# Optimization experiments

Hardware: AMD Instinct MI355X
Metric: run time of the kernel (lower is better)

The kernel has to match this reference:

```python
import jax, jax.numpy as jnp
import numpy as np

NUM_SAMPLES = 2048
MAX_AGENTS = 64
D_MODEL = 128
NUM_HEADS = 8


def setup_inputs() -> dict:
    key = jax.random.key(0)
    # deterministic ragged sizes: 1..64 repeating -> total = 32 * (64*65/2) = 66560
    agents = ((np.arange(NUM_SAMPLES) % MAX_AGENTS) + 1).astype(np.int32)
    total = int(agents.sum())
    k1, k2, k3 = jax.random.split(key, 3)
    s = 1.0 / np.sqrt(D_MODEL)
    return {
        "att_in": jax.random.normal(k1, (total, D_MODEL), jnp.float32),
        "in_proj_w": jax.random.uniform(k2, (3 * D_MODEL, D_MODEL), jnp.float32, -s, s),
        "in_proj_b": jnp.zeros((3 * D_MODEL,), jnp.float32),
        "out_proj_w": jax.random.uniform(k3, (D_MODEL, D_MODEL), jnp.float32, -s, s),
        "out_proj_b": jnp.zeros((D_MODEL,), jnp.float32),
        "agents_per_sample": jnp.asarray(agents),
    }


def reference(att_in, in_proj_w, in_proj_b, out_proj_w, out_proj_b, agents_per_sample):
    # agents_per_sample is static ragged metadata (host ints)
    agents = np.asarray(agents_per_sample)
    B = len(agents)
    A = int(agents.max())
    D = att_in.shape[-1]
    hd = D // NUM_HEADS

    # scatter ragged tokens into zero-padded [B, A, D]
    sample_ids = np.repeat(np.arange(B), agents)
    pos = np.concatenate([np.arange(n) for n in agents])
    padded = jnp.zeros((B, A, D), att_in.dtype).at[sample_ids, pos].set(att_in)
    key_valid = jnp.asarray(np.arange(A)[None, :] < agents[:, None])  # [B, A]

    # torch nn.MultiheadAttention math (eval mode, dropout=0)
    qkv = padded @ in_proj_w.T + in_proj_b  # [B, A, 3D]
    q, k, v = jnp.split(qkv, 3, axis=-1)
    q = q.reshape(B, A, NUM_HEADS, hd)
    k = k.reshape(B, A, NUM_HEADS, hd)
    v = v.reshape(B, A, NUM_HEADS, hd)

    scores = jnp.einsum("bqhd,bkhd->bhqk", q, k) / jnp.sqrt(jnp.asarray(hd, q.dtype))
    scores = jnp.where(key_valid[:, None, None, :], scores, jnp.asarray(-1e30, scores.dtype))
    attn = jax.nn.softmax(scores, axis=-1)

    out = jnp.einsum("bhqk,bkhd->bqhd", attn, v).reshape(B, A, D)
    out = out @ out_proj_w.T + out_proj_b

    # unpad: concatenation of the per-sample ragged outputs
    return out[sample_ids, pos]
```

## Files before the change

kernel.cpp:

```cpp
#include <hip/hip_runtime.h>

#define DM 128

typedef __attribute__((ext_vector_type(8))) __bf16 bf16x8;
typedef __attribute__((ext_vector_type(4))) float f32x4;

__device__ inline unsigned short f2bf(float f) {
    unsigned u = __float_as_uint(f);
    u += 0x7FFFu + ((u >> 16) & 1u);
    return (unsigned short)(u >> 16);
}

__global__ void prep(const int* __restrict__ agents, int B, int M,
                     const float* __restrict__ wqkv, const float* __restrict__ wout,
                     const float* __restrict__ x,
                     int* __restrict__ offs,
                     unsigned short* __restrict__ wqkv_bf,
                     unsigned short* __restrict__ wout_bf,
                     unsigned short* __restrict__ xbf) {
    if (blockIdx.x < 64) {
        int idx = (blockIdx.x * 256 + threadIdx.x) * 4;
        if (idx < 49152) {
            float4 v = *(const float4*)(wqkv + idx);
            ushort4 o;
            o.x = f2bf(v.x); o.y = f2bf(v.y); o.z = f2bf(v.z); o.w = f2bf(v.w);
            *(ushort4*)(wqkv_bf + idx) = o;
        } else {
            int j = idx - 49152;
            float4 v = *(const float4*)(wout + j);
            ushort4 o;
            o.x = f2bf(v.x); o.y = f2bf(v.y); o.z = f2bf(v.z); o.w = f2bf(v.w);
            *(ushort4*)(wout_bf + j) = o;
        }
    } else if (blockIdx.x == 64) {
        __shared__ int part[256];
        const int tid = threadIdx.x;
        const int per = (B + 255) >> 8;
        const int base = tid * per;
        int s = 0;
        for (int i = 0; i < per; ++i) {
            int idx = base + i;
            if (idx < B) s += agents[idx];
        }
        part[tid] = s;
        __syncthreads();
        for (int off = 1; off < 256; off <<= 1) {
            int v = (tid >= off) ? part[tid - off] : 0;
            __syncthreads();
            part[tid] += v;
            __syncthreads();
        }
        int run = (tid == 0) ? 0 : part[tid - 1];
        for (int i = 0; i < per; ++i) {
            int idx = base + i;
            if (idx < B) { offs[idx] = run; run += agents[idx]; }
        }
    } else {
        const int nf4 = M * 32;
        const int stride = ((int)gridDim.x - 65) * 256;
        for (int idx = ((int)blockIdx.x - 65) * 256 + (int)threadIdx.x; idx < nf4;
             idx += stride) {
            float4 v = ((const float4*)x)[idx];
            ushort4 o;
            o.x = f2bf(v.x); o.y = f2bf(v.y); o.z = f2bf(v.z); o.w = f2bf(v.w);
            ((ushort4*)xbf)[idx] = o;
        }
    }
}

template<int NT>
__device__ __forceinline__ void qa_body(
    const unsigned short* __restrict__ xbf,
    const unsigned short* __restrict__ wqkvb,
    const float* __restrict__ bqkv,
    unsigned short* __restrict__ obuf,
    int n, int base, int M, int h, int quad, int l16)
{
    constexpr int G   = (NT + 1) / 2;
    constexpr int KT2 = 2 * G;
    bf16x8 qf[NT], kf[NT], vA[G];
    #pragma unroll
    for (int g = 0; g < G; ++g) vA[g] = (bf16x8)(__bf16)0.0f;

    const int shA = (quad & 1) * 32 + l16;
    const int shB = shA + 16;

    #pragma unroll
    for (int seg = 0; seg < 2; ++seg) {
        bf16x8 wf[4];
        #pragma unroll
        for (int ks = 0; ks < 4; ++ks)
            wf[ks] = *(const bf16x8*)(wqkvb +
                     (size_t)(seg * 128 + h * 16 + l16) * 128 + ks * 32 + quad * 8);
        const float4 bs = *(const float4*)(bqkv + seg * 128 + h * 16 + quad * 4);
        #pragma unroll
        for (int mt = 0; mt < NT; ++mt) {
            int row = base + mt * 16 + l16;
            row = row < M ? row : M - 1;
            const unsigned short* xr = xbf + (size_t)row * 128;
            f32x4 acc = {0.f, 0.f, 0.f, 0.f};
            #pragma unroll
            for (int ks = 0; ks < 4; ++ks) {
                bf16x8 xf = *(const bf16x8*)(xr + ks * 32 + quad * 8);
                acc = __builtin_amdgcn_mfma_f32_16x16x32_bf16(wf[ks], xf, acc, 0, 0, 0);
            }
            ushort4 w;
            w.x = f2bf(acc[0] + bs.x); w.y = f2bf(acc[1] + bs.y);
            w.z = f2bf(acc[2] + bs.z); w.w = f2bf(acc[3] + bs.w);
            unsigned u0 = (unsigned)w.x | ((unsigned)w.y << 16);
            unsigned u1 = (unsigned)w.z | ((unsigned)w.w << 16);
            uint4 q;
            q.x = __shfl(u0, shA); q.y = __shfl(u1, shA);
            q.z = __shfl(u0, shB); q.w = __shfl(u1, shB);
            bf16x8 fr = (quad < 2) ? __builtin_bit_cast(bf16x8, q)
                                   : (bf16x8)(__bf16)0.0f;
            if (seg == 0) qf[mt] = fr; else kf[mt] = fr;
        }
    }
    {
        bf16x8 wfv[4];
        #pragma unroll
        for (int ks = 0; ks < 4; ++ks)
            wfv[ks] = *(const bf16x8*)(wqkvb +
                      (size_t)(256 + h * 16 + l16) * 128 + ks * 32 + quad * 8);
        const float bv = bqkv[256 + h * 16 + l16];
        #pragma unroll
        for (int t = 0; t < NT; ++t) {
            int row = base + t * 16 + l16;
            row = row < M ? row : M - 1;
            const unsigned short* xr = xbf + (size_t)row * 128;
            f32x4 acc = {0.f, 0.f, 0.f, 0.f};
            #pragma unroll
            for (int ks = 0; ks < 4; ++ks) {
                bf16x8 xf = *(const bf16x8*)(xr + ks * 32 + quad * 8);
                acc = __builtin_amdgcn_mfma_f32_16x16x32_bf16(xf, wfv[ks], acc, 0, 0, 0);
            }
            #pragma unroll
            for (int r = 0; r < 4; ++r)
                vA[t >> 1][(t & 1) * 4 + r] = (__bf16)(acc[r] + bv);
        }
    }

    __syncthreads();

    int thr[KT2];
    #pragma unroll
    for (int kt = 0; kt < KT2; ++kt) {
        int t = n - kt * 16 - quad * 4;
        thr[kt] = t < 0 ? 0 : (t > 4 ? 4 : t);
    }
    const float SC2 = 0.25f * 1.44269504088896340736f;

    #pragma unroll
    for (int mt = 0; mt < NT; ++mt) {
        float pr[KT2][4];
        float mm = -3.0e38f;
        #pragma unroll
        for (int kt = 0; kt < KT2; ++kt) {
            if (kt < NT) {
                f32x4 sc = __builtin_amdgcn_mfma_f32_16x16x32_bf16(
                    kf[kt], qf[mt], (f32x4){0.f, 0.f, 0.f, 0.f}, 0, 0, 0);
                #pragma unroll
                for (int r = 0; r < 4; ++r) {
                    float v = sc[r] * SC2;
                    pr[kt][r] = v;
                    mm = fmaxf(mm, v);
                }
            } else {
                #pragma unroll
                for (int r = 0; r < 4; ++r) pr[kt][r] = -3.0e38f;
            }
        }
        mm = fmaxf(mm, __shfl_xor(mm, 16));
        mm = fmaxf(mm, __shfl_xor(mm, 32));
        float ll = 0.f;
        #pragma unroll
        for (int kt = 0; kt < KT2; ++kt)
            #pragma unroll
            for (int r = 0; r < 4; ++r) {
                float e = exp2f(pr[kt][r] - mm);
                e = (r < thr[kt]) ? e : 0.f;
                pr[kt][r] = e;
                ll += e;
            }
        ll += __shfl_xor(ll, 16);
        ll += __shfl_xor(ll, 32);
        float inv = __builtin_amdgcn_rcpf(ll);
        bf16x8 pf[G];
        #pragma unroll
        for (int g = 0; g < G; ++g)
            #pragma unroll
            for (int j = 0; j < 8; ++j)
                pf[g][j] = (__bf16)(pr[2 * g + (j >> 2)][j & 3] * inv);
        f32x4 o = __builtin_amdgcn_mfma_f32_16x16x32_bf16(
            vA[0], pf[0], (f32x4){0.f, 0.f, 0.f, 0.f}, 0, 0, 0);
        if constexpr (G == 2)
            o = __builtin_amdgcn_mfma_f32_16x16x32_bf16(vA[1], pf[1], o, 0, 0, 0);
        const int row = mt * 16 + l16;
        if (row < n) {
            ushort4 w;
            w.x = f2bf(o[0]); w.y = f2bf(o[1]); w.z = f2bf(o[2]); w.w = f2bf(o[3]);
            *(ushort4*)(obuf + (size_t)(base + row) * 128 + h * 16 + quad * 4) = w;
        }
    }
}

__launch_bounds__(512, 2)
__global__ void qkvattn(const unsigned short* __restrict__ xbf,
                        const unsigned short* __restrict__ wqkvb,
                        const float* __restrict__ bqkv,
                        unsigned short* __restrict__ obuf,
                        const int* __restrict__ agents,
                        const int* __restrict__ offs,
                        int M) {
    const int s = blockIdx.x;
    const int n = agents[s];
    const int base = offs[s];
    const int tid = threadIdx.x;
    const int h = tid >> 6, quad = (tid >> 4) & 3, l16 = tid & 15;
    const int nt = (n + 15) >> 4;
    if      (nt == 1) qa_body<1>(xbf, wqkvb, bqkv, obuf, n, base, M, h, quad, l16);
    else if (nt == 2) qa_body<2>(xbf, wqkvb, bqkv, obuf, n, base, M, h, quad, l16);
    else if (nt == 3) qa_body<3>(xbf, wqkvb, bqkv, obuf, n, base, M, h, quad, l16);
    else              qa_body<4>(xbf, wqkvb, bqkv, obuf, n, base, M, h, quad, l16);
}

__launch_bounds__(256, 4)
__global__ void oproj(const unsigned short* __restrict__ attn_b,
                      const unsigned short* __restrict__ woutb,
                      const float* __restrict__ bout,
                      float* __restrict__ out, int M) {
    __shared__ __align__(16) unsigned short Ws[128 * 136];
    __shared__ __align__(16) float biass[128];
    const int m0 = blockIdx.x * 64;
    const int tid = threadIdx.x;

    for (int f = tid; f < 2048; f += 256) {
        int t = f >> 4, c = f & 15;
        *(uint4*)&Ws[t * 136 + c * 8] = *(const uint4*)(woutb + (size_t)t * 128 + c * 8);
    }
    if (tid < 32)
        ((float4*)biass)[tid] = ((const float4*)bout)[tid];
    __syncthreads();

    const int wave = tid >> 6, lane = tid & 63, quad = lane >> 4, l16 = lane & 15;
    const int mw = m0 + wave * 16;

    bf16x8 af[4];
    {
        int row = mw + l16;
        row = (row < M) ? row : (M - 1);
        #pragma unroll
        for (int ks = 0; ks < 4; ++ks)
            af[ks] = *(const bf16x8*)(attn_b + (size_t)row * DM + ks * 32 + quad * 8);
    }

    const int row0 = mw + l16;

    for (int ct = 0; ct < 8; ++ct) {
        bf16x8 bc[4];
        #pragma unroll
        for (int ks = 0; ks < 4; ++ks)
            bc[ks] = *(const bf16x8*)&Ws[(ct * 16 + l16) * 136 + ks * 32 + quad * 8];
        f32x4 a0 = {0.f, 0.f, 0.f, 0.f};
        #pragma unroll
        for (int ks = 0; ks < 4; ++ks)
            a0 = __builtin_amdgcn_mfma_f32_16x16x32_bf16(bc[ks], af[ks], a0, 0, 0, 0);
        const int n0 = ct * 16 + quad * 4;
        const float4 b4 = *(const float4*)(biass + n0);
        float4 o0;
        o0.x = a0[0] + b4.x; o0.y = a0[1] + b4.y; o0.z = a0[2] + b4.z; o0.w = a0[3] + b4.w;
        if (row0 < M) *(float4*)(out + (size_t)row0 * DM + n0) = o0;
    }
}

extern "C" void kernel_launch(void* const* d_in, const int* in_sizes, int n_in,
                              void* d_out, int out_size, void* d_ws, size_t ws_size,
                              hipStream_t stream) {
    const float* att_in     = (const float*)d_in[0];
    const float* in_proj_w  = (const float*)d_in[1];
    const float* in_proj_b  = (const float*)d_in[2];
    const float* out_proj_w = (const float*)d_in[3];
    const float* out_proj_b = (const float*)d_in[4];
    const int*   agents     = (const int*)d_in[5];
    const int B = in_sizes[5];
    const int M = out_size / DM;

    int* offs = (int*)d_ws;
    unsigned short* wqkv_bf = (unsigned short*)((char*)d_ws + 8192);
    unsigned short* wout_bf = (unsigned short*)((char*)d_ws + 106496);
    unsigned short* xobuf   = (unsigned short*)((char*)d_ws + 139264);

    hipLaunchKernelGGL(prep, dim3(65 + 1024), dim3(256), 0, stream,
                       agents, B, M, in_proj_w, out_proj_w, att_in,
                       offs, wqkv_bf, wout_bf, xobuf);
    hipLaunchKernelGGL(qkvattn, dim3(B), dim3(512), 0, stream,
                       xobuf, wqkv_bf, in_proj_b, xobuf, agents, offs, M);
    hipLaunchKernelGGL(oproj, dim3((M + 63) / 64), dim3(256), 0, stream,
                       xobuf, wout_bf, out_proj_b, (float*)d_out, M);
}
```

Baseline: 170.7 us.

## Split attention into per-head single-wave blocks and fuse QKV projections

The fused projection-attention kernel now launches one 64-thread block per (sample, head) instead of one 512-thread block per sample. Q, K and V are computed in a single pass over each 16-row tile, so the x fragments are loaded once and reused for all three projections. The attention output is written to a separate buffer (the output array, with a stride of 256 ushorts), so the in-place overwrite of x goes away and the block-wide barrier can be dropped. The cost is more tiny blocks, aliasing of the output buffer inside oproj, and more registers held live for the fused projection.

```diff
diff --git a/kernel.cpp b/kernel.cpp
--- a/kernel.cpp
+++ b/kernel.cpp
@@ -82,66 +82,63 @@
     #pragma unroll
     for (int g = 0; g < G; ++g) vA[g] = (bf16x8)(__bf16)0.0f;
 
+    bf16x8 wfq[4], wfk[4], wfv[4];
+    const unsigned short* wq = wqkvb + (size_t)(h * 16 + l16) * 128;
+    #pragma unroll
+    for (int ks = 0; ks < 4; ++ks) {
+        wfq[ks] = *(const bf16x8*)(wq + ks * 32 + quad * 8);
+        wfk[ks] = *(const bf16x8*)(wq + 128 * 128 + ks * 32 + quad * 8);
+        wfv[ks] = *(const bf16x8*)(wq + 256 * 128 + ks * 32 + quad * 8);
+    }
+    const float4 bq4 = *(const float4*)(bqkv + h * 16 + quad * 4);
+    const float4 bk4 = *(const float4*)(bqkv + 128 + h * 16 + quad * 4);
+    const float  bv  = bqkv[256 + h * 16 + l16];
+
     const int shA = (quad & 1) * 32 + l16;
     const int shB = shA + 16;
 
     #pragma unroll
-    for (int seg = 0; seg < 2; ++seg) {
-        bf16x8 wf[4];
-        #pragma unroll
-        for (int ks = 0; ks < 4; ++ks)
-            wf[ks] = *(const bf16x8*)(wqkvb +
-                     (size_t)(seg * 128 + h * 16 + l16) * 128 + ks * 32 + quad * 8);
-        const float4 bs = *(const float4*)(bqkv + seg * 128 + h * 16 + quad * 4);
-        #pragma unroll
-        for (int mt = 0; mt < NT; ++mt) {
-            int row = base + mt * 16 + l16;
-            row = row < M ? row : M - 1;
-            const unsigned short* xr = xbf + (size_t)row * 128;
-            f32x4 acc = {0.f, 0.f, 0.f, 0.f};
-            #pragma unroll
-            for (int ks = 0; ks < 4; ++ks) {
-                bf16x8 xf = *(const bf16x8*)(xr + ks * 32 + quad * 8);
-                acc = __builtin_amdgcn_mfma_f32_16x16x32_bf16(wf[ks], xf, acc, 0, 0, 0);
-            }
+    for (int mt = 0; mt < NT; ++mt) {
+        int row = base + mt * 16 + l16;
+        row = row < M ? row : M - 1;
+        const unsigned short* xr = xbf + (size_t)row * 128;
+        bf16x8 xf[4];
+        #pragma unroll
+        for (int ks = 0; ks < 4; ++ks)
+            xf[ks] = *(const bf16x8*)(xr + ks * 32 + quad * 8);
+        f32x4 qa = {0.f,0.f,0.f,0.f}, ka = {0.f,0.f,0.f,0.f}, va = {0.f,0.f,0.f,0.f};
+        #pragma unroll
+        for (int ks = 0; ks < 4; ++ks) {
+            qa = __builtin_amdgcn_mfma_f32_16x16x32_bf16(wfq[ks], xf[ks], qa, 0, 0, 0);
+            ka = __builtin_amdgcn_mfma_f32_16x16x32_bf16(wfk[ks], xf[ks], ka, 0, 0, 0);
+            va = __builtin_amdgcn_mfma_f32_16x16x32_bf16(xf[ks], wfv[ks], va, 0, 0, 0);
+        }
+        {
             ushort4 w;
-            w.x = f2bf(acc[0] + bs.x); w.y = f2bf(acc[1] + bs.y);
-            w.z = f2bf(acc[2] + bs.z); w.w = f2bf(acc[3] + bs.w);
+            w.x = f2bf(qa[0] + bq4.x); w.y = f2bf(qa[1] + bq4.y);
+            w.z = f2bf(qa[2] + bq4.z); w.w = f2bf(qa[3] + bq4.w);
             unsigned u0 = (unsigned)w.x | ((unsigned)w.y << 16);
             unsigned u1 = (unsigned)w.z | ((unsigned)w.w << 16);
             uint4 q;
             q.x = __shfl(u0, shA); q.y = __shfl(u1, shA);
             q.z = __shfl(u0, shB); q.w = __shfl(u1, shB);
-            bf16x8 fr = (quad < 2) ? __builtin_bit_cast(bf16x8, q)
-                                   : (bf16x8)(__bf16)0.0f;
-            if (seg == 0) qf[mt] = fr; else kf[mt] = fr;
-        }
-    }
-    {
-        bf16x8 wfv[4];
-        #pragma unroll
-        for (int ks = 0; ks < 4; ++ks)
-            wfv[ks] = *(const bf16x8*)(wqkvb +
-                      (size_t)(256 + h * 16 + l16) * 128 + ks * 32 + quad * 8);
-        const float bv = bqkv[256 + h * 16 + l16];
-        #pragma unroll
-        for (int t = 0; t < NT; ++t) {
-            int row = base + t * 16 + l16;
-            row = row < M ? row : M - 1;
-            const unsigned short* xr = xbf + (size_t)row * 128;
-            f32x4 acc = {0.f, 0.f, 0.f, 0.f};
-            #pragma unroll
-            for (int ks = 0; ks < 4; ++ks) {
-                bf16x8 xf = *(const bf16x8*)(xr + ks * 32 + quad * 8);
-                acc = __builtin_amdgcn_mfma_f32_16x16x32_bf16(xf, wfv[ks], acc, 0, 0, 0);
-            }
-            #pragma unroll
-            for (int r = 0; r < 4; ++r)
-                vA[t >> 1][(t & 1) * 4 + r] = (__bf16)(acc[r] + bv);
-        }
-    }
-
-    __syncthreads();
+            qf[mt] = (quad < 2) ? __builtin_bit_cast(bf16x8, q) : (bf16x8)(__bf16)0.0f;
+        }
+        {
+            ushort4 w;
+            w.x = f2bf(ka[0] + bk4.x); w.y = f2bf(ka[1] + bk4.y);
+            w.z = f2bf(ka[2] + bk4.z); w.w = f2bf(ka[3] + bk4.w);
+            unsigned u0 = (unsigned)w.x | ((unsigned)w.y << 16);
+            unsigned u1 = (unsigned)w.z | ((unsigned)w.w << 16);
+            uint4 q;
+            q.x = __shfl(u0, shA); q.y = __shfl(u1, shA);
+            q.z = __shfl(u0, shB); q.w = __shfl(u1, shB);
+            kf[mt] = (quad < 2) ? __builtin_bit_cast(bf16x8, q) : (bf16x8)(__bf16)0.0f;
+        }
+        #pragma unroll
+        for (int r = 0; r < 4; ++r)
+            vA[mt >> 1][(mt & 1) * 4 + r] = (__bf16)(va[r] + bv);
+    }
 
     int thr[KT2];
     #pragma unroll
@@ -200,12 +197,12 @@
         if (row < n) {
             ushort4 w;
             w.x = f2bf(o[0]); w.y = f2bf(o[1]); w.z = f2bf(o[2]); w.w = f2bf(o[3]);
-            *(ushort4*)(obuf + (size_t)(base + row) * 128 + h * 16 + quad * 4) = w;
-        }
-    }
-}
-
-__launch_bounds__(512, 2)
+            *(ushort4*)(obuf + (size_t)(base + row) * 256 + h * 16 + quad * 4) = w;
+        }
+    }
+}
+
+__launch_bounds__(64, 3)
 __global__ void qkvattn(const unsigned short* __restrict__ xbf,
                         const unsigned short* __restrict__ wqkvb,
                         const float* __restrict__ bqkv,
@@ -213,11 +210,11 @@
                         const int* __restrict__ agents,
                         const int* __restrict__ offs,
                         int M) {
-    const int s = blockIdx.x;
+    const int bid = blockIdx.x;
+    const int s = bid >> 3, h = bid & 7;
     const int n = agents[s];
     const int base = offs[s];
-    const int tid = threadIdx.x;
-    const int h = tid >> 6, quad = (tid >> 4) & 3, l16 = tid & 15;
+    const int lane = threadIdx.x & 63, quad = lane >> 4, l16 = lane & 15;
     const int nt = (n + 15) >> 4;
     if      (nt == 1) qa_body<1>(xbf, wqkvb, bqkv, obuf, n, base, M, h, quad, l16);
     else if (nt == 2) qa_body<2>(xbf, wqkvb, bqkv, obuf, n, base, M, h, quad, l16);
@@ -252,7 +249,7 @@
         row = (row < M) ? row : (M - 1);
         #pragma unroll
         for (int ks = 0; ks < 4; ++ks)
-            af[ks] = *(const bf16x8*)(attn_b + (size_t)row * DM + ks * 32 + quad * 8);
+            af[ks] = *(const bf16x8*)(attn_b + (size_t)row * 256 + ks * 32 + quad * 8);
     }
 
     const int row0 = mw + l16;
@@ -289,13 +286,14 @@
     int* offs = (int*)d_ws;
     unsigned short* wqkv_bf = (unsigned short*)((char*)d_ws + 8192);
     unsigned short* wout_bf = (unsigned short*)((char*)d_ws + 106496);
-    unsigned short* xobuf   = (unsigned short*)((char*)d_ws + 139264);
+    unsigned short* xbf     = (unsigned short*)((char*)d_ws + 139264);
+    unsigned short* obuf    = (unsigned short*)d_out;
 
     hipLaunchKernelGGL(prep, dim3(65 + 1024), dim3(256), 0, stream,
                        agents, B, M, in_proj_w, out_proj_w, att_in,
-                       offs, wqkv_bf, wout_bf, xobuf);
-    hipLaunchKernelGGL(qkvattn, dim3(B), dim3(512), 0, stream,
-                       xobuf, wqkv_bf, in_proj_b, xobuf, agents, offs, M);
+                       offs, wqkv_bf, wout_bf, xbf);
+    hipLaunchKernelGGL(qkvattn, dim3(B * 8), dim3(64), 0, stream,
+                       xbf, wqkv_bf, in_proj_b, obuf, agents, offs, M);
     hipLaunchKernelGGL(oproj, dim3((M + 63) / 64), dim3(256), 0, stream,
-                       xobuf, wout_bf, out_proj_b, (float*)d_out, M);
-}
+                       obuf, wout_bf, out_proj_b, (float*)d_out, M);
+}
```

After: 153.2 us. 1.11x faster.
